# Kernel tuning notes

Measured on AMD Instinct MI355X. Metric: run time of the kernel, lower is better.

The kernel has to match this reference:

```python
import jax, jax.numpy as jnp
import numpy as np

NUM_HEADS = 16
DIM_HEAD = 64
DIM_SEQ = 1024
DIM_INNER = NUM_HEADS * DIM_HEAD


def setup_inputs() -> dict:
    key = jax.random.key(0)
    k1, k2, k3, k4 = jax.random.split(key, 4)
    x = jax.random.normal(k1, (4, 2048, DIM_SEQ), dtype=jnp.float32)
    # nn.Linear weights stored [out, in]; apply as x @ W.T
    w_qkv = jax.random.normal(k2, (3 * DIM_INNER, DIM_SEQ), dtype=jnp.float32) * (DIM_SEQ ** -0.5)
    w_out = jax.random.normal(k3, (DIM_SEQ, DIM_INNER), dtype=jnp.float32) * (DIM_INNER ** -0.5)
    b_out = jax.random.normal(k4, (DIM_SEQ,), dtype=jnp.float32) * 0.01
    return {"x": x, "w_qkv": w_qkv, "w_out": w_out, "b_out": b_out}


def reference(x, w_qkv, w_out, b_out):
    b, n, _ = x.shape
    h, d = NUM_HEADS, DIM_HEAD
    scale = d ** -0.5
    qkv = x @ w_qkv.T  # [b, n, 3*h*d]
    q, k, v = jnp.split(qkv, 3, axis=-1)
    def to_heads(t):
        return t.reshape(b, n, h, d).transpose(0, 2, 1, 3)  # [b, h, n, d]
    q, k, v = map(to_heads, (q, k, v))
    dots = jnp.einsum('bhid,bhjd->bhij', q, k) * scale
    attn = jax.nn.softmax(dots, axis=-1)
    out = jnp.einsum('bhij,bhjd->bhid', attn, v)
    out = out.transpose(0, 2, 1, 3).reshape(b, n, h * d)
    return out @ w_out.T + b_out
```

## Files before the change

kernel.cpp:

```cpp
#include <hip/hip_runtime.h>
#include <hip/hip_bf16.h>

typedef __attribute__((ext_vector_type(8))) short bf16x8;
typedef __attribute__((ext_vector_type(4))) short shortx4;
typedef __attribute__((ext_vector_type(4))) float floatx4;
typedef __attribute__((ext_vector_type(16))) float floatx16;
typedef __attribute__((ext_vector_type(2))) unsigned uint2v;


__device__ __forceinline__ unsigned short f2b(float f) {
    union { float f; unsigned int u; } v; v.f = f;
    unsigned int r = (v.u + 0x7FFFu + ((v.u >> 16) & 1u)) >> 16;
    return (unsigned short)r;
}

__device__ __forceinline__ unsigned int cvtpk(float a, float b) {
    unsigned int r;
    asm("v_cvt_pk_bf16_f32 %0, %1, %2" : "=v"(r) : "v"(a), "v"(b));
    return r;
}

__device__ __forceinline__ void gload_lds16(const void* g, void* l) {
    __builtin_amdgcn_global_load_lds(
        (const __attribute__((address_space(1))) void*)g,
        (__attribute__((address_space(3))) void*)l, 16, 0, 0);
}

__device__ __forceinline__ float xswap32(float v) {
    uint2v r = __builtin_amdgcn_permlane32_swap(__float_as_uint(v), __float_as_uint(v), false, false);
    return __uint_as_float((threadIdx.x & 32) ? r[0] : r[1]);
}


__global__ __launch_bounds__(256) void f2b_kernel(const float* __restrict__ in,
                                                  unsigned short* __restrict__ out,
                                                  int n) {
    int i = (blockIdx.x * 256 + threadIdx.x) * 4;
    if (i >= n) return;
    floatx4 v = *(const floatx4*)&in[i];
    shortx4 o;
    o[0] = (short)f2b(v[0]); o[1] = (short)f2b(v[1]);
    o[2] = (short)f2b(v[2]); o[3] = (short)f2b(v[3]);
    *(shortx4*)&out[i] = o;
}


template <int MODE>
__global__ __launch_bounds__(256) void gemm_bt(
    const unsigned short* __restrict__ A, const unsigned short* __restrict__ B,
    int M, int N, int K,
    unsigned short* __restrict__ Qo, unsigned short* __restrict__ Ko,
    unsigned short* __restrict__ Vt,
    float* __restrict__ Cout, const float* __restrict__ bias)
{
    __shared__ unsigned short As[128 * 64];
    __shared__ unsigned short Bs[128 * 64];

    const int t = threadIdx.x;
    const int lane = t & 63, wid = t >> 6;
    const int wr = wid >> 1, wc = wid & 1;
    const int nbn = N >> 7;

    const int nwg = gridDim.x;
    const int cpx = nwg >> 3;
    const int gid = blockIdx.x;
    const int swz = (gid & 7) * cpx + (gid >> 3);
    const int m0 = (swz / nbn) << 7;
    const int n0 = (swz % nbn) << 7;

    floatx4 acc[4][4];
#pragma unroll
    for (int i = 0; i < 4; i++)
#pragma unroll
        for (int j = 0; j < 4; j++) acc[i][j] = (floatx4)0.0f;

    const int row_s = t >> 3;
    const int ch = t & 7;

    const int nkt = K >> 6;
    for (int kt = 0; kt < nkt; ++kt) {
        const int k0 = kt << 6;
#pragma unroll
        for (int it = 0; it < 4; ++it) {
            const int row = row_s + it * 32;
            gload_lds16(A + (size_t)(m0 + row) * K + k0 + ch * 8, &As[row * 64 + ch * 8]);
            gload_lds16(B + (size_t)(n0 + row) * K + k0 + ch * 8, &Bs[row * 64 + ch * 8]);
        }
        __syncthreads();
#pragma unroll
        for (int ks = 0; ks < 2; ++ks) {
            bf16x8 a[4], b[4];
#pragma unroll
            for (int i = 0; i < 4; i++)
                a[i] = *(const bf16x8*)&As[(64 * wr + 16 * i + (lane & 15)) * 64 + ks * 32 + (lane >> 4) * 8];
#pragma unroll
            for (int j = 0; j < 4; j++)
                b[j] = *(const bf16x8*)&Bs[(64 * wc + 16 * j + (lane & 15)) * 64 + ks * 32 + (lane >> 4) * 8];
#pragma unroll
            for (int i = 0; i < 4; i++)
#pragma unroll
                for (int j = 0; j < 4; j++)
                    acc[i][j] = __builtin_amdgcn_mfma_f32_16x16x32_bf16(a[i], b[j], acc[i][j], 0, 0, 0);
        }
        __syncthreads();
    }

#pragma unroll
    for (int i = 0; i < 4; i++) {
        const int mrow = m0 + 64 * wr + 16 * i + ((lane >> 4) << 2);
#pragma unroll
        for (int j = 0; j < 4; j++) {
            const int col = n0 + 64 * wc + 16 * j + (lane & 15);
            if (MODE == 0) {
                const int sel = col >> 10;
                const int h = (col >> 6) & 15;
                const int d = col & 63;
                const int bb = mrow >> 11;
                const int n = mrow & 2047;
                const int bh = bb * 16 + h;
                if (sel == 2) {
                    shortx4 v;
#pragma unroll
                    for (int r = 0; r < 4; r++) v[r] = (short)f2b(acc[i][j][r]);
                    *(shortx4*)&Vt[(size_t)(bh * 64 + d) * 2048 + n] = v;
                } else {
                    unsigned short* dst = (sel == 0 ? Qo : Ko) + (size_t)(bh * 2048 + n) * 64 + d;
#pragma unroll
                    for (int r = 0; r < 4; r++) dst[(size_t)r * 64] = f2b(acc[i][j][r]);
                }
            } else {
                const float bi = bias[col];
#pragma unroll
                for (int r = 0; r < 4; r++)
                    Cout[(size_t)(mrow + r) * N + col] = acc[i][j][r] + bi;
            }
        }
    }
}


__global__ __launch_bounds__(256) void attn_kernel(
    const unsigned short* __restrict__ Q, const unsigned short* __restrict__ Kp,
    const unsigned short* __restrict__ Vt, unsigned short* __restrict__ O)
{
    __shared__ unsigned short KV[2][2][4096];

    const int t = threadIdx.x, lane = t & 63;
    const int l31 = lane & 31, hb = lane >> 5;
    const int bid = blockIdx.x;
    const int x = bid & 7, seq = bid >> 3;
    const int head = x + 8 * (seq & 7);
    const int qb = seq >> 3;
    const size_t base_nd = (size_t)head * 2048 * 64;
    const int q0w = qb * 128 + (t >> 6) * 32;

    const int s_row = t >> 3, s_ch = t & 7;
    const int xk = (l31 & 7) << 3;
    int foff[2][4];
#pragma unroll
    for (int blk = 0; blk < 2; blk++)
#pragma unroll
        for (int dstep = 0; dstep < 4; dstep++)
            foff[blk][dstep] = (blk * 32 + l31) * 64 + ((dstep * 16 + hb * 8) ^ xk);

    const float sc = 0.18033688011112042f;

    bf16x8 qf[4];
#pragma unroll
    for (int dstep = 0; dstep < 4; dstep++) {
        union { bf16x8 v; unsigned short s[8]; unsigned u[4]; } in, ov;
        in.v = *(const bf16x8*)&Q[base_nd + (size_t)(q0w + l31) * 64 + dstep * 16 + hb * 8];
#pragma unroll
        for (int p = 0; p < 4; p++) {
            const float f0 = __uint_as_float((unsigned)in.s[2 * p] << 16) * sc;
            const float f1 = __uint_as_float((unsigned)in.s[2 * p + 1] << 16) * sc;
            ov.u[p] = cvtpk(f0, f1);
        }
        qf[dstep] = ov.v;
    }

    floatx16 o2[2];
    o2[0] = (floatx16)0.0f; o2[1] = (floatx16)0.0f;
    floatx4 l4 = (floatx4)0.0f;

#pragma unroll
    for (int rnd = 0; rnd < 2; rnd++) {
        const int row = s_row + rnd * 32;
        const int swr = (s_ch * 8) ^ ((row & 7) << 3);
        const int c = rnd * 256 + t;
        gload_lds16(Kp + base_nd + (size_t)row * 64 + swr, &KV[0][0][c * 8]);
        gload_lds16(Vt + base_nd + (size_t)row * 2048 + swr, &KV[0][1][c * 8]);
    }
    __syncthreads();

    for (int nt = 0; nt < 32; ++nt) {
        const int cur = nt & 1;
        const int ntn = (nt + 1) & 31;

#pragma unroll
        for (int rnd = 0; rnd < 2; rnd++) {
            const int row = s_row + rnd * 32;
            const int swr = (s_ch * 8) ^ ((row & 7) << 3);
            const int c = rnd * 256 + t;
            gload_lds16(Kp + base_nd + (size_t)(ntn * 64 + row) * 64 + swr, &KV[cur ^ 1][0][c * 8]);
            gload_lds16(Vt + base_nd + (size_t)row * 2048 + ntn * 64 + swr, &KV[cur ^ 1][1][c * 8]);
        }

        const unsigned short* kbuf = KV[cur][0];
        const unsigned short* vbuf = KV[cur][1];

        bf16x8 kreg[2][4];
#pragma unroll
        for (int kblk = 0; kblk < 2; kblk++)
#pragma unroll
            for (int dstep = 0; dstep < 4; dstep++)
                kreg[kblk][dstep] = *(const bf16x8*)&kbuf[foff[kblk][dstep]];

        floatx16 st[2];
        st[0] = (floatx16)0.0f; st[1] = (floatx16)0.0f;
#pragma unroll
        for (int dstep = 0; dstep < 4; dstep++) {
            st[0] = __builtin_amdgcn_mfma_f32_32x32x16_bf16(kreg[0][dstep], qf[dstep], st[0], 0, 0, 0);
            st[1] = __builtin_amdgcn_mfma_f32_32x32x16_bf16(kreg[1][dstep], qf[dstep], st[1], 0, 0, 0);
        }

#pragma unroll
        for (int kblk = 0; kblk < 2; kblk++)
#pragma unroll
            for (int i = 0; i < 16; i += 4) {
                float p0 = __builtin_amdgcn_exp2f(st[kblk][i + 0]);
                float p1 = __builtin_amdgcn_exp2f(st[kblk][i + 1]);
                float p2 = __builtin_amdgcn_exp2f(st[kblk][i + 2]);
                float p3 = __builtin_amdgcn_exp2f(st[kblk][i + 3]);
                st[kblk][i + 0] = p0; st[kblk][i + 1] = p1;
                st[kblk][i + 2] = p2; st[kblk][i + 3] = p3;
                l4[0] += p0; l4[1] += p1; l4[2] += p2; l4[3] += p3;
            }

        unsigned W[16];
#pragma unroll
        for (int kblk = 0; kblk < 2; kblk++)
#pragma unroll
            for (int q2 = 0; q2 < 4; q2++) {
                const int m = kblk * 4 + q2;
                W[2 * m]     = cvtpk(st[kblk][4 * q2 + 0], st[kblk][4 * q2 + 1]);
                W[2 * m + 1] = cvtpk(st[kblk][4 * q2 + 2], st[kblk][4 * q2 + 3]);
            }

        bf16x8 vreg[2][4];
#pragma unroll
        for (int dblk = 0; dblk < 2; dblk++)
#pragma unroll
            for (int kstep = 0; kstep < 4; kstep++)
                vreg[dblk][kstep] = *(const bf16x8*)&vbuf[foff[dblk][kstep]];

#pragma unroll
        for (int kstep = 0; kstep < 4; kstep++) {
            uint2v r0 = __builtin_amdgcn_permlane32_swap(W[4 * kstep + 0], W[4 * kstep + 2], false, false);
            uint2v r1 = __builtin_amdgcn_permlane32_swap(W[4 * kstep + 1], W[4 * kstep + 3], false, false);
            union { unsigned u[4]; bf16x8 v; } pu;
            pu.u[0] = r0[0]; pu.u[1] = r1[0]; pu.u[2] = r0[1]; pu.u[3] = r1[1];
            o2[0] = __builtin_amdgcn_mfma_f32_32x32x16_bf16(vreg[0][kstep], pu.v, o2[0], 0, 0, 0);
            o2[1] = __builtin_amdgcn_mfma_f32_32x32x16_bf16(vreg[1][kstep], pu.v, o2[1], 0, 0, 0);
        }

        __syncthreads();
    }

    const int bb = head >> 4, h = head & 15;
    const int qg = q0w + l31;
    const float l_own = (l4[0] + l4[1]) + (l4[2] + l4[3]);
    const float inv = 1.0f / (l_own + xswap32(l_own));
    unsigned short* obase = O + ((size_t)(bb * 2048 + qg)) * 1024 + h * 64 + hb * 4;
#pragma unroll
    for (int dblk = 0; dblk < 2; dblk++)
#pragma unroll
        for (int q2 = 0; q2 < 4; q2++) {
            uint2 pr;
            pr.x = cvtpk(o2[dblk][4 * q2 + 0] * inv, o2[dblk][4 * q2 + 1] * inv);
            pr.y = cvtpk(o2[dblk][4 * q2 + 2] * inv, o2[dblk][4 * q2 + 3] * inv);
            *(uint2*)(obase + dblk * 32 + q2 * 8) = pr;
        }
}


extern "C" void kernel_launch(void* const* d_in, const int* in_sizes, int n_in,
                              void* d_out, int out_size, void* d_ws, size_t ws_size,
                              hipStream_t stream) {
    const float* x     = (const float*)d_in[0];
    const float* w_qkv = (const float*)d_in[1];
    const float* w_out = (const float*)d_in[2];
    const float* b_out = (const float*)d_in[3];
    float* out = (float*)d_out;

    unsigned short* xb  = (unsigned short*)d_ws;
    unsigned short* wqb = xb  + (size_t)8192 * 1024;
    unsigned short* wob = wqb + (size_t)3072 * 1024;
    unsigned short* q   = wob + (size_t)1024 * 1024;
    unsigned short* k   = q   + (size_t)64 * 2048 * 64;
    unsigned short* vt  = k   + (size_t)64 * 2048 * 64;
    unsigned short* ob  = vt  + (size_t)64 * 2048 * 64;

    f2b_kernel<<<8192, 256, 0, stream>>>(x, xb, 8192 * 1024);
    f2b_kernel<<<3072, 256, 0, stream>>>(w_qkv, wqb, 3072 * 1024);
    f2b_kernel<<<1024, 256, 0, stream>>>(w_out, wob, 1024 * 1024);

    gemm_bt<0><<<1536, 256, 0, stream>>>(xb, wqb, 8192, 3072, 1024,
                                         q, k, vt, nullptr, nullptr);
    attn_kernel<<<1024, 256, 0, stream>>>(q, k, vt, ob);
    gemm_bt<1><<<512, 256, 0, stream>>>(ob, wob, 8192, 1024, 1024,
                                        nullptr, nullptr, nullptr, out, b_out);
}
```

Before: 296.7 us.

## Replace QKV projection GEMM with 256x256-tile 8-wave pipelined kernel

Adds a dedicated QKV projection kernel, gemm8p, with 256x256 output tiles, 512 threads (8 waves) and double-buffered LDS filled by direct global-to-LDS loads. LDS layouts are XOR-swizzled to avoid bank conflicts. The K loop runs in four phases per step, each overlapping the next stage's loads with MFMA work, using explicit vmcnt waits, barriers and setprio around the MFMA block. This is meant to raise MFMA utilisation and data reuse over the old 128x128 kernel. The cost is more registers and LDS per block, and a hand-tuned schedule that depends on the fixed problem shape.

Measured after the change: 297.6 us. About the same (+0.3%).

```diff
diff --git a/kernel.cpp b/kernel.cpp
--- a/kernel.cpp
+++ b/kernel.cpp
@@ -45,12 +45,120 @@
 }
 
 
-template <int MODE>
+#define VMC(N) asm volatile("s_waitcnt vmcnt(" #N ")" ::: "memory")
+#define SCHED0 __builtin_amdgcn_sched_barrier(0)
+
+#define GPHASE(BUF, FH, KK, STAGE_STMT, VM_STMT)                              \
+  {                                                                           \
+    bf16x8 av[4], bv[4];                                                      \
+    _Pragma("unroll") for (int i = 0; i < 4; i++)                             \
+      av[i] = *(const bf16x8*)&Al[BUF][FH][wm][i * 16 + low]                  \
+                  [((KK) * 32 + hi * 8) ^ ((low & 7) << 3)];                  \
+    _Pragma("unroll") for (int j = 0; j < 4; j++)                             \
+      bv[j] = *(const bf16x8*)&Bl[BUF][KK][wn * 64 + j * 16 + low][bswz];     \
+    STAGE_STMT;                                                               \
+    VM_STMT;                                                                  \
+    SCHED0;                                                                   \
+    __builtin_amdgcn_s_barrier();                                             \
+    SCHED0;                                                                   \
+    __builtin_amdgcn_s_setprio(1);                                            \
+    _Pragma("unroll") for (int i = 0; i < 4; i++)                             \
+      _Pragma("unroll") for (int j = 0; j < 4; j++)                           \
+        acc[(FH) * 4 + i][j] = __builtin_amdgcn_mfma_f32_16x16x32_bf16(       \
+            av[i], bv[j], acc[(FH) * 4 + i][j], 0, 0, 0);                     \
+    __builtin_amdgcn_s_setprio(0);                                            \
+    SCHED0;                                                                   \
+    __builtin_amdgcn_s_barrier();                                             \
+    SCHED0;                                                                   \
+  }
+
+__global__ __launch_bounds__(512, 2) void gemm8p(
+    const unsigned short* __restrict__ A, const unsigned short* __restrict__ B,
+    unsigned short* __restrict__ Qo, unsigned short* __restrict__ Ko,
+    unsigned short* __restrict__ Vt)
+{
+    __shared__ unsigned short Al[2][2][2][64][64];
+    __shared__ unsigned short Bl[2][2][256][32];
+
+    const int t = threadIdx.x, lane = t & 63, w = t >> 6;
+    const int low = lane & 15, hi = lane >> 4;
+    const int wm = w >> 2, wn = w & 3;
+    const int bswz = (hi ^ ((low >> 1) & 3)) * 8;
+
+    const int swz = (blockIdx.x & 7) * 48 + (blockIdx.x >> 3);
+    const int m0 = (swz / 12) << 8, n0 = (swz % 12) << 8;
+
+    floatx4 acc[8][4];
+#pragma unroll
+    for (int i = 0; i < 8; i++)
+#pragma unroll
+        for (int j = 0; j < 4; j++) acc[i][j] = (floatx4)0.0f;
+
+    auto stageA = [&](int b, int f, int kt) {
+        const int r6 = t >> 3, ch = t & 7;
+        const int sc = (ch * 8) ^ ((r6 & 7) << 3);
+#pragma unroll
+        for (int l = 0; l < 2; l++) {
+            const int gr = m0 + l * 128 + f * 64 + r6;
+            gload_lds16(A + (size_t)gr * 1024 + kt * 64 + sc, &Al[b][f][l][r6][ch * 8]);
+        }
+    };
+    auto stageB = [&](int b, int k, int kt) {
+        const int r7 = t >> 2, ch = t & 3;
+        const int c = ch ^ ((r7 >> 1) & 3);
+#pragma unroll
+        for (int l = 0; l < 2; l++) {
+            const int gr = n0 + l * 128 + r7;
+            gload_lds16(B + (size_t)gr * 1024 + kt * 64 + k * 32 + c * 8,
+                        &Bl[b][k][l * 128 + r7][ch * 8]);
+        }
+    };
+
+    stageA(0, 0, 0); stageB(0, 0, 0);
+    stageA(0, 1, 0); stageB(0, 1, 0);
+    stageA(1, 0, 1); stageB(1, 0, 1);
+    VMC(8);
+    SCHED0; __builtin_amdgcn_s_barrier(); SCHED0;
+
+    for (int T = 0; T < 16; ++T) {
+        const int buf = T & 1, nb = buf ^ 1;
+        const int k1 = (T + 1) & 15, k2 = (T + 2) & 15;
+        GPHASE(buf, 0, 0, stageA(nb, 1, k1), VMC(6));
+        GPHASE(buf, 0, 1, stageB(nb, 1, k1), (void)0);
+        GPHASE(buf, 1, 0, stageA(buf, 0, k2), (void)0);
+        GPHASE(buf, 1, 1, stageB(buf, 0, k2), VMC(8));
+    }
+
+#pragma unroll
+    for (int fi = 0; fi < 8; fi++) {
+        const int mrow = m0 + wm * 128 + fi * 16 + (hi << 2);
+#pragma unroll
+        for (int fj = 0; fj < 4; fj++) {
+            const int col = n0 + wn * 64 + fj * 16 + low;
+            const int sel = col >> 10;
+            const int h = (col >> 6) & 15;
+            const int d = col & 63;
+            const int bb = mrow >> 11;
+            const int n = mrow & 2047;
+            const int bh = bb * 16 + h;
+            if (sel == 2) {
+                shortx4 v;
+#pragma unroll
+                for (int r = 0; r < 4; r++) v[r] = (short)f2b(acc[fi][fj][r]);
+                *(shortx4*)&Vt[(size_t)(bh * 64 + d) * 2048 + n] = v;
+            } else {
+                unsigned short* dst = (sel == 0 ? Qo : Ko) + (size_t)(bh * 2048 + n) * 64 + d;
+#pragma unroll
+                for (int r = 0; r < 4; r++) dst[(size_t)r * 64] = f2b(acc[fi][fj][r]);
+            }
+        }
+    }
+}
+
+
 __global__ __launch_bounds__(256) void gemm_bt(
     const unsigned short* __restrict__ A, const unsigned short* __restrict__ B,
     int M, int N, int K,
-    unsigned short* __restrict__ Qo, unsigned short* __restrict__ Ko,
-    unsigned short* __restrict__ Vt,
     float* __restrict__ Cout, const float* __restrict__ bias)
 {
     __shared__ unsigned short As[128 * 64];
@@ -111,29 +219,10 @@
 #pragma unroll
         for (int j = 0; j < 4; j++) {
             const int col = n0 + 64 * wc + 16 * j + (lane & 15);
-            if (MODE == 0) {
-                const int sel = col >> 10;
-                const int h = (col >> 6) & 15;
-                const int d = col & 63;
-                const int bb = mrow >> 11;
-                const int n = mrow & 2047;
-                const int bh = bb * 16 + h;
-                if (sel == 2) {
-                    shortx4 v;
-#pragma unroll
-                    for (int r = 0; r < 4; r++) v[r] = (short)f2b(acc[i][j][r]);
-                    *(shortx4*)&Vt[(size_t)(bh * 64 + d) * 2048 + n] = v;
-                } else {
-                    unsigned short* dst = (sel == 0 ? Qo : Ko) + (size_t)(bh * 2048 + n) * 64 + d;
-#pragma unroll
-                    for (int r = 0; r < 4; r++) dst[(size_t)r * 64] = f2b(acc[i][j][r]);
-                }
-            } else {
-                const float bi = bias[col];
-#pragma unroll
-                for (int r = 0; r < 4; r++)
-                    Cout[(size_t)(mrow + r) * N + col] = acc[i][j][r] + bi;
-            }
+            const float bi = bias[col];
+#pragma unroll
+            for (int r = 0; r < 4; r++)
+                Cout[(size_t)(mrow + r) * N + col] = acc[i][j][r] + bi;
         }
     }
 }
@@ -305,9 +394,7 @@
     f2b_kernel<<<3072, 256, 0, stream>>>(w_qkv, wqb, 3072 * 1024);
     f2b_kernel<<<1024, 256, 0, stream>>>(w_out, wob, 1024 * 1024);
 
-    gemm_bt<0><<<1536, 256, 0, stream>>>(xb, wqb, 8192, 3072, 1024,
-                                         q, k, vt, nullptr, nullptr);
+    gemm8p<<<384, 512, 0, stream>>>(xb, wqb, q, k, vt);
     attn_kernel<<<1024, 256, 0, stream>>>(q, k, vt, ob);
-    gemm_bt<1><<<512, 256, 0, stream>>>(ob, wob, 8192, 1024, 1024,
-                                        nullptr, nullptr, nullptr, out, b_out);
-}
+    gemm_bt<<<512, 256, 0, stream>>>(ob, wob, 8192, 1024, 1024, out, b_out);
+}
```
